# Performance work log

Measured on AMD Instinct MI355X. Metric: run time of the kernel, lower is better.

Reference implementation:

```python
import jax, jax.numpy as jnp
import numpy as np

B, C, H, W = 4, 256, 64, 64
C8 = C // 8


def setup_inputs() -> dict:
    key = jax.random.key(0)
    k1, k2, k3, k4 = jax.random.split(key, 4)
    x = jax.random.normal(k1, (B, C, H, W), dtype=jnp.float32)
    # conv1d(ks=1, bias=False) projections -> plain [out, in] matrices
    Wq = jax.random.normal(k2, (C8, C), dtype=jnp.float32) * (1.0 / np.sqrt(C))
    Wk = jax.random.normal(k3, (C8, C), dtype=jnp.float32) * (1.0 / np.sqrt(C))
    Wv = jax.random.normal(k4, (C, C), dtype=jnp.float32) * (1.0 / np.sqrt(C))
    gamma = jnp.zeros((1,), dtype=jnp.float32)
    return {"x": x, "Wq": Wq, "Wk": Wk, "Wv": Wv, "gamma": gamma}


def reference(x, Wq, Wk, Wv, gamma):
    b, c, h, w = x.shape
    xf = x.reshape(b, c, h * w)                      # [B, C, N]
    f = jnp.einsum('oc,bcn->bon', Wq, xf)            # [B, C/8, N] query
    g = jnp.einsum('oc,bcn->bon', Wk, xf)            # [B, C/8, N] key
    hv = jnp.einsum('oc,bcn->bon', Wv, xf)           # [B, C,   N] value
    # scores[b,i,j] = sum_c f[b,c,i] * g[b,c,j]; softmax over dim=1 (i)
    scores = jnp.einsum('bci,bcj->bij', f, g)        # [B, N, N]
    beta = jax.nn.softmax(scores, axis=1)
    # o[b,c,j] = sum_i hv[b,c,i] * beta[b,i,j]
    o = jnp.einsum('bci,bij->bcj', hv, beta)         # [B, C, N]
    out = gamma[0] * o + xf
    return out.reshape(b, c, h, w)
```

## Files before the change

kernel.cpp:

```cpp
#include <hip/hip_runtime.h>

#define B_  4
#define C_  256
#define C8_ 32
#define N_  4096

#define TJ 128
#define KI 64
#define SPLITS 4

typedef __attribute__((ext_vector_type(8)))  short bf16x8;
typedef __attribute__((ext_vector_type(16))) float f32x16;

union FragAB { bf16x8 v; unsigned short u[8]; };

__device__ __forceinline__ unsigned short f2bf(float x) {
    unsigned u = __float_as_uint(x);
    unsigned r = u + 0x7FFFu + ((u >> 16) & 1u);
    return (unsigned short)(r >> 16);
}
__device__ __forceinline__ unsigned pack2bf(float a, float b) {
    return (unsigned)f2bf(a) | ((unsigned)f2bf(b) << 16);
}
__device__ __forceinline__ float bf2f(unsigned short h) {
    return __uint_as_float(((unsigned)h) << 16);
}

__global__ __launch_bounds__(256) void prep_w_kernel(
    const float* __restrict__ Wq, const float* __restrict__ Wk,
    const float* __restrict__ Wv, unsigned short* __restrict__ Wbf)
{
    int idx = (blockIdx.x * 256 + threadIdx.x) * 4;
    int row = idx >> 8;
    int col = idx & 255;
    const float* src; int r;
    if (row < 32)      { src = Wq; r = row;      }
    else if (row < 64) { src = Wk; r = row - 32; }
    else               { src = Wv; r = row - 64; }
    float4 v = *(const float4*)&src[r * 256 + col];
    uint2 o; o.x = pack2bf(v.x, v.y); o.y = pack2bf(v.z, v.w);
    *(uint2*)&Wbf[idx] = o;
}

__global__ __launch_bounds__(256) void prep_x_kernel(
    const float* __restrict__ x, unsigned short* __restrict__ xT)
{
    __shared__ unsigned short T[64][66];
    int t  = threadIdx.x;
    int b  = blockIdx.z;
    int c0 = blockIdx.y * 64;
    int n0 = blockIdx.x * 64;
    const float* xb = x + (size_t)b * C_ * N_;
    int n_l = t & 63, c_l = t >> 6;
#pragma unroll
    for (int q = 0; q < 16; ++q) {
        int c = c_l * 16 + q;
        T[n_l][c] = f2bf(xb[(size_t)(c0 + c) * N_ + n0 + n_l]);
    }
    __syncthreads();
    unsigned short* xTb = xT + (size_t)b * N_ * C_;
    int c_l2 = t & 63, nb = t >> 6;
#pragma unroll
    for (int q = 0; q < 16; ++q) {
        int n = nb * 16 + q;
        xTb[(size_t)(n0 + n) * C_ + c0 + c_l2] = T[n][c_l2];
    }
}

__global__ __launch_bounds__(256) void proj_mfma_kernel(
    const unsigned short* __restrict__ Wbf, const unsigned short* __restrict__ xT,
    unsigned short* __restrict__ fTg, unsigned short* __restrict__ g,
    unsigned short* __restrict__ hv)
{
    int t = threadIdx.x, w = t >> 6, lane = t & 63;
    int half = lane >> 5, l31 = lane & 31;
    int b  = blockIdx.y;
    int n0 = blockIdx.x * 32;

    const unsigned short* xb = xT + ((size_t)b * N_ + n0 + l31) * C_;
    int nm = (w < 2) ? 3 : 2;
    int mt0 = w, mt1 = w + 4, mt2 = w + 8;

    f32x16 acc[3];
#pragma unroll
    for (int a = 0; a < 3; ++a) acc[a] = (f32x16)0.f;

#pragma unroll
    for (int ks = 0; ks < 16; ++ks) {
        int kofs = ks * 16 + half * 8;
        bf16x8 bfr = *(const bf16x8*)&xb[kofs];
        bf16x8 a0 = *(const bf16x8*)&Wbf[(size_t)(mt0 * 32 + l31) * 256 + kofs];
        acc[0] = __builtin_amdgcn_mfma_f32_32x32x16_bf16(a0, bfr, acc[0], 0, 0, 0);
        bf16x8 a1 = *(const bf16x8*)&Wbf[(size_t)(mt1 * 32 + l31) * 256 + kofs];
        acc[1] = __builtin_amdgcn_mfma_f32_32x32x16_bf16(a1, bfr, acc[1], 0, 0, 0);
        if (nm == 3) {
            bf16x8 a2 = *(const bf16x8*)&Wbf[(size_t)(mt2 * 32 + l31) * 256 + kofs];
            acc[2] = __builtin_amdgcn_mfma_f32_32x32x16_bf16(a2, bfr, acc[2], 0, 0, 0);
        }
    }

    unsigned short* gb = g  + (size_t)b * C8_ * N_;
    unsigned short* hb = hv + (size_t)b * C_  * N_;
#pragma unroll
    for (int im = 0; im < 3; ++im) {
        if (im >= nm) break;
        int mt = (im == 0) ? mt0 : (im == 1) ? mt1 : mt2;
#pragma unroll
        for (int r = 0; r < 16; ++r) {
            int R = mt * 32 + (r & 3) + 8 * (r >> 2) + 4 * half;
            unsigned short v = f2bf(acc[im][r]);
            if (R < 32)       fTg[((size_t)b * N_ + n0 + l31) * 32 + R] = v;
            else if (R < 64)  gb[(size_t)(R - 32) * N_ + n0 + l31] = v;
            else              hb[(size_t)(R - 64) * N_ + n0 + l31] = v;
        }
    }
}

__global__ __launch_bounds__(256, 3) void flash_kernel(
    const unsigned short* __restrict__ fTg, const unsigned short* __restrict__ g,
    const unsigned short* __restrict__ hv, unsigned short* __restrict__ o_part,
    float* __restrict__ l_part)
{
    __shared__ unsigned short pT[2][128][72];

    int t    = threadIdx.x;
    int w    = t >> 6;
    int lane = t & 63;
    int half = lane >> 5;
    int l31  = lane & 31;

    int j0    = blockIdx.x * TJ;
    int chalf = blockIdx.y;
    int bs    = blockIdx.z;
    int b     = bs >> 2;
    int s     = bs & 3;

    const unsigned short* fb = fTg + (size_t)b * N_ * 32;
    const unsigned short* gb = g   + (size_t)b * C8_ * N_;
    const unsigned short* hrow = hv + ((size_t)b * C_ + chalf * 128 + w * 32 + l31) * N_;

    FragAB gf[2];
#pragma unroll
    for (int ks = 0; ks < 2; ++ks)
#pragma unroll
        for (int r = 0; r < 8; ++r) {
            int ch = ks * 16 + half * 8 + r;
            gf[ks].u[r] = gb[(size_t)ch * N_ + j0 + w * 32 + l31];
        }

    f32x16 acc[4];
#pragma unroll
    for (int a = 0; a < 4; ++a) acc[a] = (f32x16)0.f;
    float lacc = 0.f;

    int i_begin = s * (N_ / SPLITS);

    for (int ii = 0; ii < (N_ / SPLITS) / KI; ++ii) {
        int i0  = i_begin + ii * KI;
        int buf = ii & 1;

#pragma unroll
        for (int it = 0; it < 2; ++it) {
            f32x16 sacc = (f32x16)0.f;
#pragma unroll
            for (int ks = 0; ks < 2; ++ks) {
                bf16x8 af = *(const bf16x8*)&fb[(size_t)(i0 + it * 32 + l31) * 32
                                                + ks * 16 + half * 8];
                sacc = __builtin_amdgcn_mfma_f32_32x32x16_bf16(af, gf[ks].v, sacc, 0, 0, 0);
            }
            float p[16];
#pragma unroll
            for (int r = 0; r < 16; ++r) {
                p[r] = __expf(sacc[r]);
                lacc += p[r];
            }
            int jr = w * 32 + l31;
#pragma unroll
            for (int a = 0; a < 4; ++a) {
                uint2 v;
                v.x = pack2bf(p[4 * a + 0], p[4 * a + 1]);
                v.y = pack2bf(p[4 * a + 2], p[4 * a + 3]);
                *(uint2*)&pT[buf][jr][it * 32 + 8 * a + 4 * half] = v;
            }
        }
        __syncthreads();

#pragma unroll
        for (int ks4 = 0; ks4 < 4; ++ks4) {
            int kofs = ks4 * 16 + half * 8;
            bf16x8 a = *(const bf16x8*)&hrow[i0 + kofs];
            bf16x8 bfr[4];
#pragma unroll
            for (int jt = 0; jt < 4; ++jt)
                bfr[jt] = *(const bf16x8*)&pT[buf][jt * 32 + l31][kofs];
#pragma unroll
            for (int jt = 0; jt < 4; ++jt)
                acc[jt] = __builtin_amdgcn_mfma_f32_32x32x16_bf16(a, bfr[jt], acc[jt], 0, 0, 0);
        }
    }

    unsigned short* ob = o_part + (size_t)bs * C_ * N_;
#pragma unroll
    for (int jt = 0; jt < 4; ++jt) {
        f32x16 a = acc[jt];
#pragma unroll
        for (int r = 0; r < 16; ++r) {
            int c = chalf * 128 + w * 32 + (r & 3) + 8 * (r >> 2) + 4 * half;
            int j = j0 + jt * 32 + l31;
            ob[(size_t)c * N_ + j] = f2bf(a[r]);
        }
    }
    if (chalf == 0) {
        float lsum = lacc + __shfl_down(lacc, 32);
        if (lane < 32)
            l_part[(size_t)bs * N_ + j0 + w * 32 + lane] = lsum;
    }
}

__global__ __launch_bounds__(256) void combine_kernel(
    const unsigned short* __restrict__ o_part, const float* __restrict__ l_part,
    const float* __restrict__ x, const float* __restrict__ gamma,
    float* __restrict__ out)
{
    int j = blockIdx.x * 256 + threadIdx.x;
    int b = blockIdx.z;
    float l = 0.f;
#pragma unroll
    for (int s = 0; s < SPLITS; ++s)
        l += l_part[(size_t)(b * SPLITS + s) * N_ + j];
    float inv = 1.f / l;
    float gm = gamma[0];
#pragma unroll
    for (int cc = 0; cc < 4; ++cc) {
        int c = blockIdx.y * 4 + cc;
        float o = 0.f;
#pragma unroll
        for (int s = 0; s < SPLITS; ++s)
            o += bf2f(o_part[((size_t)(b * SPLITS + s) * C_ + c) * N_ + j]);
        size_t idx = ((size_t)b * C_ + c) * N_ + j;
        out[idx] = gm * o * inv + x[idx];
    }
}

extern "C" void kernel_launch(void* const* d_in, const int* in_sizes, int n_in,
                              void* d_out, int out_size, void* d_ws, size_t ws_size,
                              hipStream_t stream) {
    const float* x     = (const float*)d_in[0];
    const float* Wq    = (const float*)d_in[1];
    const float* Wk    = (const float*)d_in[2];
    const float* Wv    = (const float*)d_in[3];
    const float* gamma = (const float*)d_in[4];
    float* out = (float*)d_out;

    char* ws = (char*)d_ws;
    unsigned short* o_part = (unsigned short*)ws;
    float* l_part = (float*)(o_part + (size_t)SPLITS * B_ * C_ * N_);
    unsigned short* fTg = (unsigned short*)(l_part + (size_t)SPLITS * B_ * N_);
    unsigned short* g   = fTg + (size_t)B_ * C8_ * N_;
    unsigned short* hv  = g   + (size_t)B_ * C8_ * N_;
    unsigned short* Wbf = hv  + (size_t)B_ * C_  * N_;
    unsigned short* xT  = Wbf + (size_t)(C_ + 2 * C8_) * C_;

    prep_w_kernel<<<dim3(80), 256, 0, stream>>>(Wq, Wk, Wv, Wbf);
    prep_x_kernel<<<dim3(N_ / 64, C_ / 64, B_), 256, 0, stream>>>(x, xT);

    proj_mfma_kernel<<<dim3(N_ / 32, B_), 256, 0, stream>>>(Wbf, xT, fTg, g, hv);

    flash_kernel<<<dim3(N_ / TJ, 2, SPLITS * B_), 256, 0, stream>>>(
        fTg, g, hv, o_part, l_part);

    combine_kernel<<<dim3(N_ / 256, C_ / 4, B_), 256, 0, stream>>>(o_part, l_part, x, gamma, out);
}
```

Before: 166.1 us.

## Restructure flash kernel to cover all channels per block and stage values in LDS

Each block of the flash kernel now handles all 256 value channels for 64 query columns instead of splitting channels across two blocks. This stops the score and exp work from being computed twice. The value tile is loaded coalesced per thread into a transposed LDS buffer, and scores use the 16x16x32 MFMA. The LDS buffer is no longer double-buffered, so each iteration needs two barriers. Tiles are smaller (TJ 64, KI 32), which may cut per-barrier work and global load efficiency.

```diff
diff --git a/kernel.cpp b/kernel.cpp
--- a/kernel.cpp
+++ b/kernel.cpp
@@ -5,11 +5,12 @@
 #define C8_ 32
 #define N_  4096
 
-#define TJ 128
-#define KI 64
+#define TJ 64
+#define KI 32
 #define SPLITS 4
 
 typedef __attribute__((ext_vector_type(8)))  short bf16x8;
+typedef __attribute__((ext_vector_type(4)))  float f32x4;
 typedef __attribute__((ext_vector_type(16))) float f32x16;
 
 union FragAB { bf16x8 v; unsigned short u[8]; };
@@ -121,32 +122,30 @@
     const unsigned short* __restrict__ hv, unsigned short* __restrict__ o_part,
     float* __restrict__ l_part)
 {
-    __shared__ unsigned short pT[2][128][72];
+    __shared__ unsigned short hvT[256][40];
+    __shared__ unsigned short pT[64][40];
 
     int t    = threadIdx.x;
     int w    = t >> 6;
     int lane = t & 63;
     int half = lane >> 5;
     int l31  = lane & 31;
-
-    int j0    = blockIdx.x * TJ;
-    int chalf = blockIdx.y;
-    int bs    = blockIdx.z;
-    int b     = bs >> 2;
-    int s     = bs & 3;
+    int q16  = lane >> 4;
+    int l15  = lane & 15;
+
+    int j0 = blockIdx.x * TJ;
+    int s  = blockIdx.y;
+    int b  = blockIdx.z;
+    int bs = b * SPLITS + s;
 
     const unsigned short* fb = fTg + (size_t)b * N_ * 32;
     const unsigned short* gb = g   + (size_t)b * C8_ * N_;
-    const unsigned short* hrow = hv + ((size_t)b * C_ + chalf * 128 + w * 32 + l31) * N_;
-
-    FragAB gf[2];
-#pragma unroll
-    for (int ks = 0; ks < 2; ++ks)
-#pragma unroll
-        for (int r = 0; r < 8; ++r) {
-            int ch = ks * 16 + half * 8 + r;
-            gf[ks].u[r] = gb[(size_t)ch * N_ + j0 + w * 32 + l31];
-        }
+    const unsigned short* hr = hv  + ((size_t)b * C_ + t) * N_;
+
+    FragAB gf;
+#pragma unroll
+    for (int r = 0; r < 8; ++r)
+        gf.u[r] = gb[(size_t)(q16 * 8 + r) * N_ + j0 + w * 16 + l15];
 
     f32x16 acc[4];
 #pragma unroll
@@ -156,65 +155,75 @@
     int i_begin = s * (N_ / SPLITS);
 
     for (int ii = 0; ii < (N_ / SPLITS) / KI; ++ii) {
-        int i0  = i_begin + ii * KI;
-        int buf = ii & 1;
-
-#pragma unroll
-        for (int it = 0; it < 2; ++it) {
-            f32x16 sacc = (f32x16)0.f;
-#pragma unroll
-            for (int ks = 0; ks < 2; ++ks) {
-                bf16x8 af = *(const bf16x8*)&fb[(size_t)(i0 + it * 32 + l31) * 32
-                                                + ks * 16 + half * 8];
-                sacc = __builtin_amdgcn_mfma_f32_32x32x16_bf16(af, gf[ks].v, sacc, 0, 0, 0);
-            }
-            float p[16];
-#pragma unroll
-            for (int r = 0; r < 16; ++r) {
+        int i0 = i_begin + ii * KI;
+
+        uint4 sv[4];
+#pragma unroll
+        for (int q = 0; q < 4; ++q)
+            sv[q] = *(const uint4*)&hr[i0 + q * 8];
+
+#pragma unroll
+        for (int mt = 0; mt < 2; ++mt) {
+            bf16x8 af = *(const bf16x8*)&fb[(size_t)(i0 + mt * 16 + l15) * 32 + q16 * 8];
+            f32x4 sacc = __builtin_amdgcn_mfma_f32_16x16x32_bf16(
+                af, gf.v, (f32x4)0.f, 0, 0, 0);
+            float p[4];
+#pragma unroll
+            for (int r = 0; r < 4; ++r) {
                 p[r] = __expf(sacc[r]);
                 lacc += p[r];
             }
-            int jr = w * 32 + l31;
-#pragma unroll
-            for (int a = 0; a < 4; ++a) {
-                uint2 v;
-                v.x = pack2bf(p[4 * a + 0], p[4 * a + 1]);
-                v.y = pack2bf(p[4 * a + 2], p[4 * a + 3]);
-                *(uint2*)&pT[buf][jr][it * 32 + 8 * a + 4 * half] = v;
+            uint2 v;
+            v.x = pack2bf(p[0], p[1]);
+            v.y = pack2bf(p[2], p[3]);
+            *(uint2*)&pT[w * 16 + l15][mt * 16 + q16 * 4] = v;
+        }
+
+#pragma unroll
+        for (int q = 0; q < 4; ++q)
+            *(uint4*)&hvT[t][q * 8] = sv[q];
+
+        __syncthreads();
+
+#pragma unroll
+        for (int ks = 0; ks < 2; ++ks) {
+            int kofs = ks * 16 + half * 8;
+            bf16x8 af[2], bfr[2];
+#pragma unroll
+            for (int ct = 0; ct < 2; ++ct)
+                af[ct] = *(const bf16x8*)&hvT[w * 64 + ct * 32 + l31][kofs];
+#pragma unroll
+            for (int jt = 0; jt < 2; ++jt)
+                bfr[jt] = *(const bf16x8*)&pT[jt * 32 + l31][kofs];
+#pragma unroll
+            for (int ct = 0; ct < 2; ++ct)
+#pragma unroll
+                for (int jt = 0; jt < 2; ++jt)
+                    acc[ct * 2 + jt] = __builtin_amdgcn_mfma_f32_32x32x16_bf16(
+                        af[ct], bfr[jt], acc[ct * 2 + jt], 0, 0, 0);
+        }
+
+        __syncthreads();
+    }
+
+    unsigned short* ob = o_part + (size_t)bs * C_ * N_;
+#pragma unroll
+    for (int ct = 0; ct < 2; ++ct)
+#pragma unroll
+        for (int jt = 0; jt < 2; ++jt) {
+            f32x16 a = acc[ct * 2 + jt];
+#pragma unroll
+            for (int r = 0; r < 16; ++r) {
+                int c = w * 64 + ct * 32 + (r & 3) + 8 * (r >> 2) + 4 * half;
+                int j = j0 + jt * 32 + l31;
+                ob[(size_t)c * N_ + j] = f2bf(a[r]);
             }
         }
-        __syncthreads();
-
-#pragma unroll
-        for (int ks4 = 0; ks4 < 4; ++ks4) {
-            int kofs = ks4 * 16 + half * 8;
-            bf16x8 a = *(const bf16x8*)&hrow[i0 + kofs];
-            bf16x8 bfr[4];
-#pragma unroll
-            for (int jt = 0; jt < 4; ++jt)
-                bfr[jt] = *(const bf16x8*)&pT[buf][jt * 32 + l31][kofs];
-#pragma unroll
-            for (int jt = 0; jt < 4; ++jt)
-                acc[jt] = __builtin_amdgcn_mfma_f32_32x32x16_bf16(a, bfr[jt], acc[jt], 0, 0, 0);
-        }
-    }
-
-    unsigned short* ob = o_part + (size_t)bs * C_ * N_;
-#pragma unroll
-    for (int jt = 0; jt < 4; ++jt) {
-        f32x16 a = acc[jt];
-#pragma unroll
-        for (int r = 0; r < 16; ++r) {
-            int c = chalf * 128 + w * 32 + (r & 3) + 8 * (r >> 2) + 4 * half;
-            int j = j0 + jt * 32 + l31;
-            ob[(size_t)c * N_ + j] = f2bf(a[r]);
-        }
-    }
-    if (chalf == 0) {
-        float lsum = lacc + __shfl_down(lacc, 32);
-        if (lane < 32)
-            l_part[(size_t)bs * N_ + j0 + w * 32 + lane] = lsum;
-    }
+    float lsum = lacc;
+    lsum += __shfl_xor(lsum, 16);
+    lsum += __shfl_xor(lsum, 32);
+    if (lane < 16)
+        l_part[(size_t)bs * N_ + j0 + w * 16 + lane] = lsum;
 }
 
 __global__ __launch_bounds__(256) void combine_kernel(
@@ -266,7 +275,7 @@
 
     proj_mfma_kernel<<<dim3(N_ / 32, B_), 256, 0, stream>>>(Wbf, xT, fTg, g, hv);
 
-    flash_kernel<<<dim3(N_ / TJ, 2, SPLITS * B_), 256, 0, stream>>>(
+    flash_kernel<<<dim3(N_ / TJ, SPLITS, B_), 256, 0, stream>>>(
         fTg, g, hv, o_part, l_part);
 
     combine_kernel<<<dim3(N_ / 256, C_ / 4, B_), 256, 0, stream>>>(o_part, l_part, x, gamma, out);
```

After: 192.7 us. 1.16x slower.

## Restructure flash kernel: register-resident P via lane shuffles, hv staged in swizzled LDS

Applied to the files above, without the earlier changes.

The flash kernel no longer splits channels across two blocks. Each block now covers all 256 channels for 128 columns, with warps tiled 2x2 over channels and columns, so the score and exp work is no longer duplicated per channel half. The softmax probabilities stay in registers and are rearranged into MFMA B-fragments with cross-half lane shuffles instead of going through LDS. The hv tile is loaded cooperatively and transposed into XOR-swizzled shared memory. In exchange, register use rises (8 accumulators, occupancy hint lowered to 2) and each iteration gains two barriers.

```diff
diff --git a/kernel.cpp b/kernel.cpp
--- a/kernel.cpp
+++ b/kernel.cpp
@@ -5,14 +5,13 @@
 #define C8_ 32
 #define N_  4096
 
-#define TJ 128
 #define KI 64
 #define SPLITS 4
 
 typedef __attribute__((ext_vector_type(8)))  short bf16x8;
 typedef __attribute__((ext_vector_type(16))) float f32x16;
 
-union FragAB { bf16x8 v; unsigned short u[8]; };
+union FragAB { bf16x8 v; unsigned short u[8]; unsigned u32[4]; };
 
 __device__ __forceinline__ unsigned short f2bf(float x) {
     unsigned u = __float_as_uint(x);
@@ -116,104 +115,138 @@
     }
 }
 
-__global__ __launch_bounds__(256, 3) void flash_kernel(
+__global__ __launch_bounds__(256, 2) void flash_kernel(
     const unsigned short* __restrict__ fTg, const unsigned short* __restrict__ g,
     const unsigned short* __restrict__ hv, unsigned short* __restrict__ o_part,
     float* __restrict__ l_part)
 {
-    __shared__ unsigned short pT[2][128][72];
+    __shared__ unsigned short hvT[256][64];
 
     int t    = threadIdx.x;
     int w    = t >> 6;
     int lane = t & 63;
     int half = lane >> 5;
     int l31  = lane & 31;
-
-    int j0    = blockIdx.x * TJ;
-    int chalf = blockIdx.y;
-    int bs    = blockIdx.z;
-    int b     = bs >> 2;
-    int s     = bs & 3;
+    int cg   = w >> 1;
+    int jg   = w & 1;
+
+    int j0 = blockIdx.x * 128;
+    int s  = blockIdx.y;
+    int b  = blockIdx.z;
+    int bs = b * SPLITS + s;
+    int jb = j0 + jg * 64;
 
     const unsigned short* fb = fTg + (size_t)b * N_ * 32;
     const unsigned short* gb = g   + (size_t)b * C8_ * N_;
-    const unsigned short* hrow = hv + ((size_t)b * C_ + chalf * 128 + w * 32 + l31) * N_;
-
-    FragAB gf[2];
-#pragma unroll
-    for (int ks = 0; ks < 2; ++ks)
-#pragma unroll
-        for (int r = 0; r < 8; ++r) {
-            int ch = ks * 16 + half * 8 + r;
-            gf[ks].u[r] = gb[(size_t)ch * N_ + j0 + w * 32 + l31];
-        }
-
-    f32x16 acc[4];
-#pragma unroll
-    for (int a = 0; a < 4; ++a) acc[a] = (f32x16)0.f;
-    float lacc = 0.f;
+    const unsigned short* hb = hv  + (size_t)b * C_ * N_;
+
+    int su = t & 7;
+    int sc0 = t >> 3;
+    int ssw = su ^ (sc0 & 7);
+
+    FragAB gf[2][2];
+#pragma unroll
+    for (int jt = 0; jt < 2; ++jt)
+#pragma unroll
+        for (int ks = 0; ks < 2; ++ks)
+#pragma unroll
+            for (int r = 0; r < 8; ++r)
+                gf[jt][ks].u[r] = gb[(size_t)(ks * 16 + half * 8 + r) * N_
+                                     + jb + jt * 32 + l31];
+
+    f32x16 acc[4][2];
+#pragma unroll
+    for (int a = 0; a < 4; ++a)
+#pragma unroll
+        for (int j = 0; j < 2; ++j) acc[a][j] = (f32x16)0.f;
+    float lacc[2] = {0.f, 0.f};
 
     int i_begin = s * (N_ / SPLITS);
 
     for (int ii = 0; ii < (N_ / SPLITS) / KI; ++ii) {
-        int i0  = i_begin + ii * KI;
-        int buf = ii & 1;
+        int i0 = i_begin + ii * KI;
+
+        uint4 sv[8];
+#pragma unroll
+        for (int rep = 0; rep < 8; ++rep)
+            sv[rep] = *(const uint4*)&hb[(size_t)(sc0 + 32 * rep) * N_ + i0 + su * 8];
+
+        __syncthreads();
+#pragma unroll
+        for (int rep = 0; rep < 8; ++rep)
+            *(uint4*)&hvT[sc0 + 32 * rep][ssw * 8] = sv[rep];
+        __syncthreads();
 
 #pragma unroll
         for (int it = 0; it < 2; ++it) {
-            f32x16 sacc = (f32x16)0.f;
-#pragma unroll
-            for (int ks = 0; ks < 2; ++ks) {
-                bf16x8 af = *(const bf16x8*)&fb[(size_t)(i0 + it * 32 + l31) * 32
-                                                + ks * 16 + half * 8];
-                sacc = __builtin_amdgcn_mfma_f32_32x32x16_bf16(af, gf[ks].v, sacc, 0, 0, 0);
+            bf16x8 af0 = *(const bf16x8*)&fb[(size_t)(i0 + it * 32 + l31) * 32 + half * 8];
+            bf16x8 af1 = *(const bf16x8*)&fb[(size_t)(i0 + it * 32 + l31) * 32 + 16 + half * 8];
+            FragAB pf[2][2];
+#pragma unroll
+            for (int jt = 0; jt < 2; ++jt) {
+                f32x16 sacc = __builtin_amdgcn_mfma_f32_32x32x16_bf16(
+                    af0, gf[jt][0].v, (f32x16)0.f, 0, 0, 0);
+                sacc = __builtin_amdgcn_mfma_f32_32x32x16_bf16(
+                    af1, gf[jt][1].v, sacc, 0, 0, 0);
+                float p[16];
+#pragma unroll
+                for (int r = 0; r < 16; ++r) {
+                    p[r] = __expf(sacc[r]);
+                    lacc[jt] += p[r];
+                }
+                unsigned o[8], e[8];
+#pragma unroll
+                for (int q = 0; q < 8; ++q) {
+                    o[q] = pack2bf(p[2 * q], p[2 * q + 1]);
+                    e[q] = __shfl_xor((int)o[q], 32);
+                }
+#pragma unroll
+                for (int kb = 0; kb < 2; ++kb) {
+                    pf[jt][kb].u32[0] = half ? e[4 * kb + 2] : o[4 * kb + 0];
+                    pf[jt][kb].u32[1] = half ? e[4 * kb + 3] : o[4 * kb + 1];
+                    pf[jt][kb].u32[2] = half ? o[4 * kb + 2] : e[4 * kb + 0];
+                    pf[jt][kb].u32[3] = half ? o[4 * kb + 3] : e[4 * kb + 1];
+                }
             }
-            float p[16];
+#pragma unroll
+            for (int kb = 0; kb < 2; ++kb) {
+                int unit = (it * 2 + kb) * 2 + half;
+                bf16x8 afr[4];
+#pragma unroll
+                for (int ct = 0; ct < 4; ++ct) {
+                    int c = cg * 128 + ct * 32 + l31;
+                    afr[ct] = *(const bf16x8*)&hvT[c][(unit ^ (c & 7)) * 8];
+                }
+#pragma unroll
+                for (int ct = 0; ct < 4; ++ct)
+#pragma unroll
+                    for (int jt = 0; jt < 2; ++jt)
+                        acc[ct][jt] = __builtin_amdgcn_mfma_f32_32x32x16_bf16(
+                            afr[ct], pf[jt][kb].v, acc[ct][jt], 0, 0, 0);
+            }
+        }
+    }
+
+    unsigned short* ob = o_part + (size_t)bs * C_ * N_;
+#pragma unroll
+    for (int ct = 0; ct < 4; ++ct)
+#pragma unroll
+        for (int jt = 0; jt < 2; ++jt) {
+            f32x16 a = acc[ct][jt];
 #pragma unroll
             for (int r = 0; r < 16; ++r) {
-                p[r] = __expf(sacc[r]);
-                lacc += p[r];
+                int c = cg * 128 + ct * 32 + (r & 3) + 8 * (r >> 2) + 4 * half;
+                int j = jb + jt * 32 + l31;
+                ob[(size_t)c * N_ + j] = f2bf(a[r]);
             }
-            int jr = w * 32 + l31;
-#pragma unroll
-            for (int a = 0; a < 4; ++a) {
-                uint2 v;
-                v.x = pack2bf(p[4 * a + 0], p[4 * a + 1]);
-                v.y = pack2bf(p[4 * a + 2], p[4 * a + 3]);
-                *(uint2*)&pT[buf][jr][it * 32 + 8 * a + 4 * half] = v;
-            }
-        }
-        __syncthreads();
-
-#pragma unroll
-        for (int ks4 = 0; ks4 < 4; ++ks4) {
-            int kofs = ks4 * 16 + half * 8;
-            bf16x8 a = *(const bf16x8*)&hrow[i0 + kofs];
-            bf16x8 bfr[4];
-#pragma unroll
-            for (int jt = 0; jt < 4; ++jt)
-                bfr[jt] = *(const bf16x8*)&pT[buf][jt * 32 + l31][kofs];
-#pragma unroll
-            for (int jt = 0; jt < 4; ++jt)
-                acc[jt] = __builtin_amdgcn_mfma_f32_32x32x16_bf16(a, bfr[jt], acc[jt], 0, 0, 0);
-        }
-    }
-
-    unsigned short* ob = o_part + (size_t)bs * C_ * N_;
-#pragma unroll
-    for (int jt = 0; jt < 4; ++jt) {
-        f32x16 a = acc[jt];
-#pragma unroll
-        for (int r = 0; r < 16; ++r) {
-            int c = chalf * 128 + w * 32 + (r & 3) + 8 * (r >> 2) + 4 * half;
-            int j = j0 + jt * 32 + l31;
-            ob[(size_t)c * N_ + j] = f2bf(a[r]);
-        }
-    }
-    if (chalf == 0) {
-        float lsum = lacc + __shfl_down(lacc, 32);
-        if (lane < 32)
-            l_part[(size_t)bs * N_ + j0 + w * 32 + lane] = lsum;
+        }
+    if (cg == 0) {
+#pragma unroll
+        for (int jt = 0; jt < 2; ++jt) {
+            float lsum = lacc[jt] + __shfl_xor(lacc[jt], 32);
+            if (half == 0)
+                l_part[(size_t)bs * N_ + jb + jt * 32 + l31] = lsum;
+        }
     }
 }
 
@@ -266,7 +299,7 @@
 
     proj_mfma_kernel<<<dim3(N_ / 32, B_), 256, 0, stream>>>(Wbf, xT, fTg, g, hv);
 
-    flash_kernel<<<dim3(N_ / TJ, 2, SPLITS * B_), 256, 0, stream>>>(
+    flash_kernel<<<dim3(N_ / 128, SPLITS, B_), 256, 0, stream>>>(
         fTg, g, hv, o_part, l_part);
 
     combine_kernel<<<dim3(N_ / 256, C_ / 4, B_), 256, 0, stream>>>(o_part, l_part, x, gamma, out);
```

New measurement: 235.7 us. +41.9%, slower.
